# Kernel tuning notes

Hardware: AMD Instinct MI355X
Metric: run time of the kernel (lower is better)

## Reference

```python
import jax, jax.numpy as jnp
import numpy as np

MAX_SEQ_LEN = 2048
H, K = 16, 8
D_IN, D_OUT = 1024, 1024
D_H, D_O = D_IN // H, D_OUT // H


def _get_phi(L, K):
    # Hankel matrix Z[i,j] = 2 / ((i+j)^3 - (i+j) + 1e-7), 1-indexed
    e = np.arange(1, L + 1, dtype=np.float64)
    s = e[:, None] + e[None, :]
    Z = 2.0 / (s ** 3 - s + 1e-7)
    sigma, phi = np.linalg.eigh(Z)
    sigma, phi = sigma[-K:], phi[:, -K:]
    phi = phi * sigma ** 0.25
    return jnp.asarray(phi, dtype=jnp.float32)  # (L, K)


def setup_inputs() -> dict:
    key = jax.random.key(0)
    k_x, k_w, k_d = jax.random.split(key, 3)
    B, T = 4, 2048
    x = jax.random.normal(k_x, (B, T, D_IN), dtype=jnp.float32)
    # kaiming_uniform(a=sqrt(5)) on (H,K,d_h,d_o): fan_in = K*d_h*d_o, bound = 1/sqrt(fan_in)
    fan_in = K * D_H * D_O
    bound = 1.0 / np.sqrt(fan_in)
    weight = jax.random.uniform(k_w, (H, K, D_H, D_O), minval=-bound, maxval=bound, dtype=jnp.float32)
    # torch init is zeros; use small random so the score path is exercised
    diag = 0.02 * jax.random.normal(k_d, (K, D_IN), dtype=jnp.float32)
    phi = _get_phi(MAX_SEQ_LEN, K)
    return {"x": x, "weight": weight, "diag": diag, "phi": phi}


def reference(x, weight, diag, phi):
    B, T, _ = x.shape
    Hh, Kk, d_h, d_o = weight.shape
    # scores: (B, T, K) = phi[:T] broadcast + x @ diag^T
    scores = phi[:T][None, :, :] + jnp.einsum('bti,ki->btk', x, diag)
    xh = x.reshape(B, T, Hh, d_h).transpose(0, 2, 1, 3)  # (B, H, T, d_h)
    # per-head, per-expert GEMM -> (B, H, K, T, d_o)
    y = jnp.einsum('bhti,hkio->bhkto', xh, weight)
    # score-weighted combine over experts -> (B, T, H, d_o)
    y = jnp.einsum('bhkto,btk->btho', y, scores)
    return y.reshape(B, T, Hh * d_o)
```

## Files before the change

kernel.cpp:

```cpp
#include <hip/hip_runtime.h>
#include <hip/hip_bf16.h>

#define BT    8192
#define SEQ_T 2048
#define DIN   1024
#define NH    16
#define NK    8
#define DH    64
#define DO    64

typedef __bf16 bf16;
typedef __attribute__((ext_vector_type(8))) __bf16 bf16x8;
typedef __attribute__((ext_vector_type(4))) __bf16 bf16x4;
typedef __attribute__((ext_vector_type(4))) float floatx4;

__global__ __launch_bounds__(256) void prep_kernel(
    const float* __restrict__ x, const float* __restrict__ weight,
    const float* __restrict__ diag, const float* __restrict__ phi,
    float* __restrict__ scores_t, bf16* __restrict__ wt)
{
  int blk = blockIdx.x, tid = threadIdx.x;
  if (blk < BT / 4) {
    int wave = tid >> 6, lane = tid & 63;
    int token = blk * 4 + wave;
    const floatx4* xr = (const floatx4*)(x + (size_t)token * DIN);
    const floatx4* dg = (const floatx4*)diag;
    floatx4 acc[NK];
#pragma unroll
    for (int k = 0; k < NK; k++) acc[k] = (floatx4){0.f, 0.f, 0.f, 0.f};
#pragma unroll
    for (int it = 0; it < 4; it++) {
      floatx4 xv = xr[it * 64 + lane];
#pragma unroll
      for (int k = 0; k < NK; k++) {
        floatx4 dv = dg[k * 256 + it * 64 + lane];
        acc[k] += xv * dv;
      }
    }
    float r[NK];
#pragma unroll
    for (int k = 0; k < NK; k++)
      r[k] = (acc[k][0] + acc[k][1]) + (acc[k][2] + acc[k][3]);
#pragma unroll
    for (int k = 0; k < NK; k++) {
      float v = r[k];
#pragma unroll
      for (int off = 32; off >= 1; off >>= 1) v += __shfl_xor(v, off, 64);
      r[k] = v;
    }
    if (lane == 0) {
      int t = token & (SEQ_T - 1);
#pragma unroll
      for (int k = 0; k < NK; k++)
        scores_t[(size_t)k * BT + token] = phi[t * NK + k] + r[k];
    }
  } else {
    __shared__ bf16 tile[64 * 68];
    int hk = blk - BT / 4;
    const float* wsrc = weight + (size_t)hk * DH * DO;
#pragma unroll
    for (int it = 0; it < 4; it++) {
      int idx = it * 1024 + tid * 4;
      int i = idx >> 6, o = idx & 63;
      floatx4 v = *(const floatx4*)(wsrc + idx);
#pragma unroll
      for (int r = 0; r < 4; r++)
        tile[(o + r) * 68 + i] = (bf16)v[r];
    }
    __syncthreads();
#pragma unroll
    for (int it = 0; it < 4; it++) {
      int idx = it * 1024 + tid * 4;
      int o2 = idx >> 6, i2 = idx & 63;
      bf16x4 v = *(const bf16x4*)&tile[o2 * 68 + i2];
      *(bf16x4*)(wt + (size_t)hk * 4096 + idx) = v;
    }
  }
}

__global__ __launch_bounds__(256, 3) void moe_kernel(
    const float* __restrict__ x, const bf16* __restrict__ wt,
    const float* __restrict__ scores_t, float* __restrict__ out)
{
  __shared__ bf16  xl[128 * 64];
  __shared__ bf16  wl[256 * 64];
  __shared__ float sl[NK * 128];

  int bid = blockIdx.x;
  int g  = bid >> 5;
  int h  = (bid >> 1) & 15;
  int nh = bid & 1;
  int tid = threadIdx.x, lane = tid & 63, w = tid >> 6;
  int l15 = lane & 15, q = lane >> 4;

  {
    const float* xs = x + (size_t)(g * 128) * DIN + h * 64;
#pragma unroll
    for (int it = 0; it < 4; it++) {
      int idx = it * 256 + tid;
      int row = idx >> 3, c = idx & 7;
      const float* p = xs + (size_t)row * DIN + c * 8;
      floatx4 u0 = *(const floatx4*)p;
      floatx4 u1 = *(const floatx4*)(p + 4);
      bf16x8 v;
      v[0] = (bf16)u0[0]; v[1] = (bf16)u0[1];
      v[2] = (bf16)u0[2]; v[3] = (bf16)u0[3];
      v[4] = (bf16)u1[0]; v[5] = (bf16)u1[1];
      v[6] = (bf16)u1[2]; v[7] = (bf16)u1[3];
      int pc = c ^ (row & 7);
      *(bf16x8*)(xl + row * 64 + pc * 8) = v;
    }
  }
  {
#pragma unroll
    for (int it = 0; it < 8; it++) {
      int idx = it * 256 + tid;
      int R = idx >> 3, c = idx & 7;
      int e = R >> 5, o = R & 31;
      bf16x8 v = *(const bf16x8*)(wt + ((size_t)(h * NK + e) * DO + nh * 32 + o) * 64 + c * 8);
      int pc = c ^ (R & 7);
      *(bf16x8*)(wl + R * 64 + pc * 8) = v;
    }
  }
  {
    int k = tid >> 5, t4 = (tid & 31) * 4;
    floatx4 v = *(const floatx4*)(scores_t + (size_t)k * BT + g * 128 + t4);
    *(floatx4*)(sl + k * 128 + t4) = v;
  }
  __syncthreads();

  int mh = w >> 1;
  int ns = w & 1;

  bf16x8 b[NK][2];
#pragma unroll
  for (int e = 0; e < NK; e++) {
    int R = e * 32 + ns * 16 + l15;
#pragma unroll
    for (int ki = 0; ki < 2; ki++) {
      int pc = (ki * 4 + q) ^ (R & 7);
      b[e][ki] = *(const bf16x8*)(wl + R * 64 + pc * 8);
    }
  }

#pragma unroll
  for (int m = 0; m < 4; m++) {
    int tr = mh * 64 + m * 16;
    int row = tr + l15;
    int p0 = q ^ (row & 7), p1 = (q + 4) ^ (row & 7);
    bf16x8 a0 = *(const bf16x8*)(xl + row * 64 + p0 * 8);
    bf16x8 a1 = *(const bf16x8*)(xl + row * 64 + p1 * 8);
    floatx4 y = (floatx4){0.f, 0.f, 0.f, 0.f};
#pragma unroll
    for (int e = 0; e < NK; e++) {
      floatx4 s4 = *(const floatx4*)(sl + e * 128 + tr + q * 4);
      floatx4 z = (floatx4){0.f, 0.f, 0.f, 0.f};
      z = __builtin_amdgcn_mfma_f32_16x16x32_bf16(a0, b[e][0], z, 0, 0, 0);
      z = __builtin_amdgcn_mfma_f32_16x16x32_bf16(a1, b[e][1], z, 0, 0, 0);
      y += s4 * z;
    }
    int orow = g * 128 + tr + q * 4;
    float* op = out + (size_t)orow * (NH * DO) + h * DO + nh * 32 + ns * 16 + l15;
#pragma unroll
    for (int r = 0; r < 4; r++)
      op[(size_t)r * (NH * DO)] = y[r];
  }
}

extern "C" void kernel_launch(void* const* d_in, const int* in_sizes, int n_in,
                              void* d_out, int out_size, void* d_ws, size_t ws_size,
                              hipStream_t stream) {
  const float* x      = (const float*)d_in[0];
  const float* weight = (const float*)d_in[1];
  const float* diag   = (const float*)d_in[2];
  const float* phi    = (const float*)d_in[3];
  float* out = (float*)d_out;

  bf16*  wt       = (bf16*)d_ws;
  float* scores_t = (float*)((char*)d_ws + (2u << 20));

  prep_kernel<<<BT / 4 + NH * NK, 256, 0, stream>>>(x, weight, diag, phi,
                                                    scores_t, wt);
  moe_kernel<<<64 * NH * 2, 256, 0, stream>>>(x, wt, scores_t, out);
}
```

Before: 110.0 us.

## Fuse prep and MoE kernels into one persistent kernel with grid barrier

Merges the score/weight-prep kernel and the MoE GEMM kernel into one persistent kernel of 768 blocks. Blocks grid-stride over the score tokens and weight-transpose tiles, meet at an atomic-counter grid barrier, then grid-stride over the GEMM tiles. The aim is to remove the second launch and the gap between the kernels. In exchange it adds a memset, a software grid barrier that assumes all 768 blocks are resident at once (256 CUs × 3), and less parallelism in the GEMM phase, since each block now handles about 1.3 tiles sequentially.

```diff
diff --git a/kernel.cpp b/kernel.cpp
--- a/kernel.cpp
+++ b/kernel.cpp
@@ -8,21 +8,43 @@
 #define NK    8
 #define DH    64
 #define DO    64
+#define GRID  768
 
 typedef __bf16 bf16;
 typedef __attribute__((ext_vector_type(8))) __bf16 bf16x8;
 typedef __attribute__((ext_vector_type(4))) __bf16 bf16x4;
 typedef __attribute__((ext_vector_type(4))) float floatx4;
 
-__global__ __launch_bounds__(256) void prep_kernel(
+__device__ __forceinline__ void grid_sync(unsigned* cnt) {
+  __syncthreads();
+  if (threadIdx.x == 0) {
+    __threadfence();
+    unsigned v = __hip_atomic_fetch_add(cnt, 1u, __ATOMIC_ACQ_REL,
+                                        __HIP_MEMORY_SCOPE_AGENT);
+    unsigned target = (v / GRID + 1u) * GRID;
+    while (__hip_atomic_load(cnt, __ATOMIC_ACQUIRE,
+                             __HIP_MEMORY_SCOPE_AGENT) < target)
+      __builtin_amdgcn_s_sleep(2);
+    __threadfence();
+  }
+  __syncthreads();
+}
+
+__global__ __launch_bounds__(256, 3) void fused_kernel(
     const float* __restrict__ x, const float* __restrict__ weight,
     const float* __restrict__ diag, const float* __restrict__ phi,
-    float* __restrict__ scores_t, bf16* __restrict__ wt)
+    bf16* __restrict__ wt, float* __restrict__ scores_t,
+    float* __restrict__ out, unsigned* __restrict__ cnt)
 {
-  int blk = blockIdx.x, tid = threadIdx.x;
-  if (blk < BT / 4) {
-    int wave = tid >> 6, lane = tid & 63;
-    int token = blk * 4 + wave;
+  __shared__ bf16  xl[128 * 64];
+  __shared__ bf16  wl[256 * 64];
+  __shared__ float sl[NK * 128];
+
+  int b = blockIdx.x, tid = threadIdx.x;
+  int wave = tid >> 6, lane = tid & 63;
+
+  for (int tq = b; tq < BT / 4; tq += GRID) {
+    int token = tq * 4 + wave;
     const floatx4* xr = (const floatx4*)(x + (size_t)token * DIN);
     const floatx4* dg = (const floatx4*)diag;
     floatx4 acc[NK];
@@ -54,10 +76,11 @@
       for (int k = 0; k < NK; k++)
         scores_t[(size_t)k * BT + token] = phi[t * NK + k] + r[k];
     }
-  } else {
-    __shared__ bf16 tile[64 * 68];
-    int hk = blk - BT / 4;
-    const float* wsrc = weight + (size_t)hk * DH * DO;
+  }
+
+  if (b < NH * NK) {
+    bf16* tile = wl;
+    const float* wsrc = weight + (size_t)b * DH * DO;
 #pragma unroll
     for (int it = 0; it < 4; it++) {
       int idx = it * 1024 + tid * 4;
@@ -73,97 +96,92 @@
       int idx = it * 1024 + tid * 4;
       int o2 = idx >> 6, i2 = idx & 63;
       bf16x4 v = *(const bf16x4*)&tile[o2 * 68 + i2];
-      *(bf16x4*)(wt + (size_t)hk * 4096 + idx) = v;
-    }
-  }
-}
-
-__global__ __launch_bounds__(256, 3) void moe_kernel(
-    const float* __restrict__ x, const bf16* __restrict__ wt,
-    const float* __restrict__ scores_t, float* __restrict__ out)
-{
-  __shared__ bf16  xl[128 * 64];
-  __shared__ bf16  wl[256 * 64];
-  __shared__ float sl[NK * 128];
-
-  int bid = blockIdx.x;
-  int g  = bid >> 5;
-  int h  = (bid >> 1) & 15;
-  int nh = bid & 1;
-  int tid = threadIdx.x, lane = tid & 63, w = tid >> 6;
-  int l15 = lane & 15, q = lane >> 4;
-
-  {
-    const float* xs = x + (size_t)(g * 128) * DIN + h * 64;
-#pragma unroll
-    for (int it = 0; it < 4; it++) {
-      int idx = it * 256 + tid;
-      int row = idx >> 3, c = idx & 7;
-      const float* p = xs + (size_t)row * DIN + c * 8;
-      floatx4 u0 = *(const floatx4*)p;
-      floatx4 u1 = *(const floatx4*)(p + 4);
-      bf16x8 v;
-      v[0] = (bf16)u0[0]; v[1] = (bf16)u0[1];
-      v[2] = (bf16)u0[2]; v[3] = (bf16)u0[3];
-      v[4] = (bf16)u1[0]; v[5] = (bf16)u1[1];
-      v[6] = (bf16)u1[2]; v[7] = (bf16)u1[3];
-      int pc = c ^ (row & 7);
-      *(bf16x8*)(xl + row * 64 + pc * 8) = v;
-    }
-  }
-  {
-#pragma unroll
-    for (int it = 0; it < 8; it++) {
-      int idx = it * 256 + tid;
-      int R = idx >> 3, c = idx & 7;
-      int e = R >> 5, o = R & 31;
-      bf16x8 v = *(const bf16x8*)(wt + ((size_t)(h * NK + e) * DO + nh * 32 + o) * 64 + c * 8);
-      int pc = c ^ (R & 7);
-      *(bf16x8*)(wl + R * 64 + pc * 8) = v;
-    }
-  }
-  {
-    int k = tid >> 5, t4 = (tid & 31) * 4;
-    floatx4 v = *(const floatx4*)(scores_t + (size_t)k * BT + g * 128 + t4);
-    *(floatx4*)(sl + k * 128 + t4) = v;
-  }
-  __syncthreads();
-
+      *(bf16x4*)(wt + (size_t)b * 4096 + idx) = v;
+    }
+  }
+
+  grid_sync(cnt);
+
+  int l15 = lane & 15, q = lane >> 4, w = tid >> 6;
   int mh = w >> 1;
   int ns = w & 1;
 
-  bf16x8 b[NK][2];
-#pragma unroll
-  for (int e = 0; e < NK; e++) {
-    int R = e * 32 + ns * 16 + l15;
-#pragma unroll
-    for (int ki = 0; ki < 2; ki++) {
-      int pc = (ki * 4 + q) ^ (R & 7);
-      b[e][ki] = *(const bf16x8*)(wl + R * 64 + pc * 8);
-    }
-  }
-
-#pragma unroll
-  for (int m = 0; m < 4; m++) {
-    int tr = mh * 64 + m * 16;
-    int row = tr + l15;
-    int p0 = q ^ (row & 7), p1 = (q + 4) ^ (row & 7);
-    bf16x8 a0 = *(const bf16x8*)(xl + row * 64 + p0 * 8);
-    bf16x8 a1 = *(const bf16x8*)(xl + row * 64 + p1 * 8);
-    floatx4 y = (floatx4){0.f, 0.f, 0.f, 0.f};
+  for (int t5 = b; t5 < 64 * NH * 2; t5 += GRID) {
+    int g  = t5 >> 5;
+    int h  = (t5 >> 1) & 15;
+    int nh = t5 & 1;
+
+    __syncthreads();
+
+    {
+      const float* xs = x + (size_t)(g * 128) * DIN + h * 64;
+#pragma unroll
+      for (int it = 0; it < 4; it++) {
+        int idx = it * 256 + tid;
+        int row = idx >> 3, c = idx & 7;
+        const float* p = xs + (size_t)row * DIN + c * 8;
+        floatx4 u0 = *(const floatx4*)p;
+        floatx4 u1 = *(const floatx4*)(p + 4);
+        bf16x8 v;
+        v[0] = (bf16)u0[0]; v[1] = (bf16)u0[1];
+        v[2] = (bf16)u0[2]; v[3] = (bf16)u0[3];
+        v[4] = (bf16)u1[0]; v[5] = (bf16)u1[1];
+        v[6] = (bf16)u1[2]; v[7] = (bf16)u1[3];
+        int pc = c ^ (row & 7);
+        *(bf16x8*)(xl + row * 64 + pc * 8) = v;
+      }
+    }
+    {
+#pragma unroll
+      for (int it = 0; it < 8; it++) {
+        int idx = it * 256 + tid;
+        int R = idx >> 3, c = idx & 7;
+        int e = R >> 5, o = R & 31;
+        bf16x8 v = *(const bf16x8*)(wt + ((size_t)(h * NK + e) * DO + nh * 32 + o) * 64 + c * 8);
+        int pc = c ^ (R & 7);
+        *(bf16x8*)(wl + R * 64 + pc * 8) = v;
+      }
+    }
+    {
+      int k = tid >> 5, t4 = (tid & 31) * 4;
+      floatx4 v = *(const floatx4*)(scores_t + (size_t)k * BT + g * 128 + t4);
+      *(floatx4*)(sl + k * 128 + t4) = v;
+    }
+    __syncthreads();
+
+    bf16x8 bfr[NK][2];
 #pragma unroll
     for (int e = 0; e < NK; e++) {
-      floatx4 s4 = *(const floatx4*)(sl + e * 128 + tr + q * 4);
-      floatx4 z = (floatx4){0.f, 0.f, 0.f, 0.f};
-      z = __builtin_amdgcn_mfma_f32_16x16x32_bf16(a0, b[e][0], z, 0, 0, 0);
-      z = __builtin_amdgcn_mfma_f32_16x16x32_bf16(a1, b[e][1], z, 0, 0, 0);
-      y += s4 * z;
-    }
-    int orow = g * 128 + tr + q * 4;
-    float* op = out + (size_t)orow * (NH * DO) + h * DO + nh * 32 + ns * 16 + l15;
-#pragma unroll
-    for (int r = 0; r < 4; r++)
-      op[(size_t)r * (NH * DO)] = y[r];
+      int R = e * 32 + ns * 16 + l15;
+#pragma unroll
+      for (int ki = 0; ki < 2; ki++) {
+        int pc = (ki * 4 + q) ^ (R & 7);
+        bfr[e][ki] = *(const bf16x8*)(wl + R * 64 + pc * 8);
+      }
+    }
+
+#pragma unroll
+    for (int m = 0; m < 4; m++) {
+      int tr = mh * 64 + m * 16;
+      int row = tr + l15;
+      int p0 = q ^ (row & 7), p1 = (q + 4) ^ (row & 7);
+      bf16x8 a0 = *(const bf16x8*)(xl + row * 64 + p0 * 8);
+      bf16x8 a1 = *(const bf16x8*)(xl + row * 64 + p1 * 8);
+      floatx4 y = (floatx4){0.f, 0.f, 0.f, 0.f};
+#pragma unroll
+      for (int e = 0; e < NK; e++) {
+        floatx4 s4 = *(const floatx4*)(sl + e * 128 + tr + q * 4);
+        floatx4 z = (floatx4){0.f, 0.f, 0.f, 0.f};
+        z = __builtin_amdgcn_mfma_f32_16x16x32_bf16(a0, bfr[e][0], z, 0, 0, 0);
+        z = __builtin_amdgcn_mfma_f32_16x16x32_bf16(a1, bfr[e][1], z, 0, 0, 0);
+        y += s4 * z;
+      }
+      int orow = g * 128 + tr + q * 4;
+      float* op = out + (size_t)orow * (NH * DO) + h * DO + nh * 32 + ns * 16 + l15;
+#pragma unroll
+      for (int r = 0; r < 4; r++)
+        op[(size_t)r * (NH * DO)] = y[r];
+    }
   }
 }
 
@@ -176,10 +194,11 @@
   const float* phi    = (const float*)d_in[3];
   float* out = (float*)d_out;
 
-  bf16*  wt       = (bf16*)d_ws;
-  float* scores_t = (float*)((char*)d_ws + (2u << 20));
-
-  prep_kernel<<<BT / 4 + NH * NK, 256, 0, stream>>>(x, weight, diag, phi,
-                                                    scores_t, wt);
-  moe_kernel<<<64 * NH * 2, 256, 0, stream>>>(x, wt, scores_t, out);
+  bf16*     wt       = (bf16*)d_ws;
+  float*    scores_t = (float*)((char*)d_ws + (2u << 20));
+  unsigned* cnt      = (unsigned*)((char*)d_ws + (3u << 20));
+
+  hipMemsetAsync(cnt, 0, 64, stream);
+  fused_kernel<<<GRID, 256, 0, stream>>>(x, weight, diag, phi, wt, scores_t,
+                                         out, cnt);
 }
```

Measured after the change: 248.2 us. +125.6%, slower.

## Fuse score computation into MoE kernel and pre-swizzle weights for direct LDS loads

Applied to the files above, without the earlier changes.

Moves the per-token score GEMV out of the prep kernel and into the main kernel, so each block of 64 tokens computes its own scores into shared memory. Each block then loops over four heads and two output halves. The weight image is written in a pre-swizzled layout, which lets it be copied straight into LDS with global_load_lds. This removes the scores round-trip through global memory and the heavy prep pass over x. The cost is that each block now runs serially: the score phase (x is read again here) and then eight sequential weight loads with syncs and no overlap. Only 512 blocks are launched, which lowers parallelism and occupancy.

```diff
diff --git a/kernel.cpp b/kernel.cpp
--- a/kernel.cpp
+++ b/kernel.cpp
@@ -14,156 +14,180 @@
 typedef __attribute__((ext_vector_type(4))) __bf16 bf16x4;
 typedef __attribute__((ext_vector_type(4))) float floatx4;
 
-__global__ __launch_bounds__(256) void prep_kernel(
-    const float* __restrict__ x, const float* __restrict__ weight,
-    const float* __restrict__ diag, const float* __restrict__ phi,
-    float* __restrict__ scores_t, bf16* __restrict__ wt)
+#define GLOAD_LDS16(gp, lp)                                        \
+  __builtin_amdgcn_global_load_lds(                                \
+      (__attribute__((address_space(1))) const void*)(gp),         \
+      (__attribute__((address_space(3))) void*)(lp), 16, 0, 0)
+
+__global__ __launch_bounds__(256) void wtrans_kernel(
+    const float* __restrict__ weight, bf16* __restrict__ wimg)
 {
-  int blk = blockIdx.x, tid = threadIdx.x;
-  if (blk < BT / 4) {
-    int wave = tid >> 6, lane = tid & 63;
-    int token = blk * 4 + wave;
-    const floatx4* xr = (const floatx4*)(x + (size_t)token * DIN);
-    const floatx4* dg = (const floatx4*)diag;
-    floatx4 acc[NK];
-#pragma unroll
-    for (int k = 0; k < NK; k++) acc[k] = (floatx4){0.f, 0.f, 0.f, 0.f};
-#pragma unroll
-    for (int it = 0; it < 4; it++) {
-      floatx4 xv = xr[it * 64 + lane];
-#pragma unroll
-      for (int k = 0; k < NK; k++) {
-        floatx4 dv = dg[k * 256 + it * 64 + lane];
-        acc[k] += xv * dv;
-      }
-    }
-    float r[NK];
-#pragma unroll
-    for (int k = 0; k < NK; k++)
-      r[k] = (acc[k][0] + acc[k][1]) + (acc[k][2] + acc[k][3]);
-#pragma unroll
-    for (int k = 0; k < NK; k++) {
-      float v = r[k];
-#pragma unroll
-      for (int off = 32; off >= 1; off >>= 1) v += __shfl_xor(v, off, 64);
-      r[k] = v;
-    }
-    if (lane == 0) {
-      int t = token & (SEQ_T - 1);
-#pragma unroll
-      for (int k = 0; k < NK; k++)
-        scores_t[(size_t)k * BT + token] = phi[t * NK + k] + r[k];
-    }
-  } else {
-    __shared__ bf16 tile[64 * 68];
-    int hk = blk - BT / 4;
-    const float* wsrc = weight + (size_t)hk * DH * DO;
-#pragma unroll
-    for (int it = 0; it < 4; it++) {
-      int idx = it * 1024 + tid * 4;
-      int i = idx >> 6, o = idx & 63;
-      floatx4 v = *(const floatx4*)(wsrc + idx);
-#pragma unroll
-      for (int r = 0; r < 4; r++)
-        tile[(o + r) * 68 + i] = (bf16)v[r];
-    }
-    __syncthreads();
-#pragma unroll
-    for (int it = 0; it < 4; it++) {
-      int idx = it * 1024 + tid * 4;
-      int o2 = idx >> 6, i2 = idx & 63;
-      bf16x4 v = *(const bf16x4*)&tile[o2 * 68 + i2];
-      *(bf16x4*)(wt + (size_t)hk * 4096 + idx) = v;
-    }
+  __shared__ bf16 tile[64 * 68];
+  int hk = blockIdx.x, tid = threadIdx.x;
+  int h = hk >> 3, k = hk & 7;
+  const float* wsrc = weight + (size_t)hk * DH * DO;
+#pragma unroll
+  for (int it = 0; it < 4; it++) {
+    int idx = it * 1024 + tid * 4;
+    int i = idx >> 6, o = idx & 63;
+    floatx4 v = *(const floatx4*)(wsrc + idx);
+#pragma unroll
+    for (int r = 0; r < 4; r++)
+      tile[(o + r) * 68 + i] = (bf16)v[r];
+  }
+  __syncthreads();
+#pragma unroll
+  for (int it = 0; it < 4; it++) {
+    int idx = it * 1024 + tid * 4;
+    int o2 = idx >> 6, i2 = idx & 63;
+    bf16x4 v = *(const bf16x4*)&tile[o2 * 68 + i2];
+    int nh = o2 >> 5, o = o2 & 31, R = k * 32 + o;
+    int a = (((i2 >> 3) ^ (R & 7)) << 3) + (i2 & 7);
+    *(bf16x4*)(wimg + ((size_t)(h * 2 + nh) * 256 + R) * 64 + a) = v;
   }
 }
 
-__global__ __launch_bounds__(256, 3) void moe_kernel(
-    const float* __restrict__ x, const bf16* __restrict__ wt,
-    const float* __restrict__ scores_t, float* __restrict__ out)
+__global__ __launch_bounds__(256, 2) void fused_kernel(
+    const float* __restrict__ x, const float* __restrict__ diag,
+    const float* __restrict__ phi, const bf16* __restrict__ wimg,
+    float* __restrict__ out)
 {
-  __shared__ bf16  xl[128 * 64];
+  __shared__ bf16  xl[64 * 64];
   __shared__ bf16  wl[256 * 64];
-  __shared__ float sl[NK * 128];
+  __shared__ float sl[NK * 64];
 
   int bid = blockIdx.x;
-  int g  = bid >> 5;
-  int h  = (bid >> 1) & 15;
-  int nh = bid & 1;
+  int lid = ((bid & 7) << 6) | (bid >> 3);
+  int g64 = lid >> 2;
+  int hq  = lid & 3;
   int tid = threadIdx.x, lane = tid & 63, w = tid >> 6;
   int l15 = lane & 15, q = lane >> 4;
 
   {
-    const float* xs = x + (size_t)(g * 128) * DIN + h * 64;
-#pragma unroll
-    for (int it = 0; it < 4; it++) {
-      int idx = it * 256 + tid;
-      int row = idx >> 3, c = idx & 7;
-      const float* p = xs + (size_t)row * DIN + c * 8;
-      floatx4 u0 = *(const floatx4*)p;
-      floatx4 u1 = *(const floatx4*)(p + 4);
-      bf16x8 v;
-      v[0] = (bf16)u0[0]; v[1] = (bf16)u0[1];
-      v[2] = (bf16)u0[2]; v[3] = (bf16)u0[3];
-      v[4] = (bf16)u1[0]; v[5] = (bf16)u1[1];
-      v[6] = (bf16)u1[2]; v[7] = (bf16)u1[3];
-      int pc = c ^ (row & 7);
-      *(bf16x8*)(xl + row * 64 + pc * 8) = v;
-    }
-  }
-  {
-#pragma unroll
-    for (int it = 0; it < 8; it++) {
-      int idx = it * 256 + tid;
-      int R = idx >> 3, c = idx & 7;
-      int e = R >> 5, o = R & 31;
-      bf16x8 v = *(const bf16x8*)(wt + ((size_t)(h * NK + e) * DO + nh * 32 + o) * 64 + c * 8);
-      int pc = c ^ (R & 7);
-      *(bf16x8*)(wl + R * 64 + pc * 8) = v;
-    }
-  }
-  {
-    int k = tid >> 5, t4 = (tid & 31) * 4;
-    floatx4 v = *(const floatx4*)(scores_t + (size_t)k * BT + g * 128 + t4);
-    *(floatx4*)(sl + k * 128 + t4) = v;
+    const floatx4* dg  = (const floatx4*)diag;
+    const floatx4* xr0 = (const floatx4*)(x + (size_t)(g64 * 64 + w * 16) * DIN);
+    floatx4 xv[4];
+#pragma unroll
+    for (int it = 0; it < 4; it++) xv[it] = xr0[it * 64 + lane];
+    for (int s = 0; s < 16; s++) {
+      floatx4 nx[4];
+      if (s < 15) {
+        const floatx4* nr = xr0 + (size_t)(s + 1) * (DIN / 4);
+#pragma unroll
+        for (int it = 0; it < 4; it++) nx[it] = nr[it * 64 + lane];
+      }
+      floatx4 acc[NK];
+#pragma unroll
+      for (int k = 0; k < NK; k++) acc[k] = (floatx4){0.f, 0.f, 0.f, 0.f};
+#pragma unroll
+      for (int it = 0; it < 4; it++) {
+#pragma unroll
+        for (int k = 0; k < NK; k++)
+          acc[k] += xv[it] * dg[k * 256 + it * 64 + lane];
+      }
+      float r[NK];
+#pragma unroll
+      for (int k = 0; k < NK; k++)
+        r[k] = (acc[k][0] + acc[k][1]) + (acc[k][2] + acc[k][3]);
+#pragma unroll
+      for (int k = 0; k < NK; k++) {
+        float v = r[k];
+#pragma unroll
+        for (int off = 32; off >= 1; off >>= 1) v += __shfl_xor(v, off, 64);
+        r[k] = v;
+      }
+      if (lane == 0) {
+        int tl = w * 16 + s;
+        int t = (g64 * 64 + tl) & (SEQ_T - 1);
+#pragma unroll
+        for (int k = 0; k < NK; k++)
+          sl[k * 64 + tl] = phi[t * NK + k] + r[k];
+      }
+      if (s < 15) {
+#pragma unroll
+        for (int it = 0; it < 4; it++) xv[it] = nx[it];
+      }
+    }
   }
   __syncthreads();
 
   int mh = w >> 1;
   int ns = w & 1;
 
-  bf16x8 b[NK][2];
-#pragma unroll
-  for (int e = 0; e < NK; e++) {
-    int R = e * 32 + ns * 16 + l15;
-#pragma unroll
-    for (int ki = 0; ki < 2; ki++) {
-      int pc = (ki * 4 + q) ^ (R & 7);
-      b[e][ki] = *(const bf16x8*)(wl + R * 64 + pc * 8);
-    }
-  }
-
-#pragma unroll
-  for (int m = 0; m < 4; m++) {
-    int tr = mh * 64 + m * 16;
-    int row = tr + l15;
-    int p0 = q ^ (row & 7), p1 = (q + 4) ^ (row & 7);
-    bf16x8 a0 = *(const bf16x8*)(xl + row * 64 + p0 * 8);
-    bf16x8 a1 = *(const bf16x8*)(xl + row * 64 + p1 * 8);
-    floatx4 y = (floatx4){0.f, 0.f, 0.f, 0.f};
+  auto compute_store = [&](int h, int nh) {
+    bf16x8 b[NK][2];
 #pragma unroll
     for (int e = 0; e < NK; e++) {
-      floatx4 s4 = *(const floatx4*)(sl + e * 128 + tr + q * 4);
-      floatx4 z = (floatx4){0.f, 0.f, 0.f, 0.f};
-      z = __builtin_amdgcn_mfma_f32_16x16x32_bf16(a0, b[e][0], z, 0, 0, 0);
-      z = __builtin_amdgcn_mfma_f32_16x16x32_bf16(a1, b[e][1], z, 0, 0, 0);
-      y += s4 * z;
-    }
-    int orow = g * 128 + tr + q * 4;
-    float* op = out + (size_t)orow * (NH * DO) + h * DO + nh * 32 + ns * 16 + l15;
-#pragma unroll
-    for (int r = 0; r < 4; r++)
-      op[(size_t)r * (NH * DO)] = y[r];
+      int R = e * 32 + ns * 16 + l15;
+#pragma unroll
+      for (int ki = 0; ki < 2; ki++) {
+        int pc = (ki * 4 + q) ^ (R & 7);
+        b[e][ki] = *(const bf16x8*)(wl + R * 64 + pc * 8);
+      }
+    }
+#pragma unroll
+    for (int m = 0; m < 2; m++) {
+      int tr = mh * 32 + m * 16;
+      int row = tr + l15;
+      int p0 = q ^ (row & 7), p1 = (q + 4) ^ (row & 7);
+      bf16x8 a0 = *(const bf16x8*)(xl + row * 64 + p0 * 8);
+      bf16x8 a1 = *(const bf16x8*)(xl + row * 64 + p1 * 8);
+      floatx4 y = (floatx4){0.f, 0.f, 0.f, 0.f};
+#pragma unroll
+      for (int e = 0; e < NK; e++) {
+        floatx4 s4 = *(const floatx4*)(sl + e * 64 + tr + q * 4);
+        floatx4 z = (floatx4){0.f, 0.f, 0.f, 0.f};
+        z = __builtin_amdgcn_mfma_f32_16x16x32_bf16(a0, b[e][0], z, 0, 0, 0);
+        z = __builtin_amdgcn_mfma_f32_16x16x32_bf16(a1, b[e][1], z, 0, 0, 0);
+        y += s4 * z;
+      }
+      int orow = g64 * 64 + tr + q * 4;
+      float* op = out + (size_t)orow * (NH * DO) + h * DO + nh * 32
+                      + ns * 16 + l15;
+#pragma unroll
+      for (int r = 0; r < 4; r++)
+        op[(size_t)r * (NH * DO)] = y[r];
+    }
+  };
+
+  for (int hh = 0; hh < 4; hh++) {
+    int h = hq * 4 + hh;
+    if (hh) __syncthreads();
+
+    {
+      const float* xs = x + (size_t)(g64 * 64) * DIN + h * 64;
+#pragma unroll
+      for (int it = 0; it < 2; it++) {
+        int idx = it * 256 + tid;
+        int row = idx >> 3, c = idx & 7;
+        const float* p = xs + (size_t)row * DIN + c * 8;
+        floatx4 u0 = *(const floatx4*)p;
+        floatx4 u1 = *(const floatx4*)(p + 4);
+        bf16x8 v;
+        v[0] = (bf16)u0[0]; v[1] = (bf16)u0[1];
+        v[2] = (bf16)u0[2]; v[3] = (bf16)u0[3];
+        v[4] = (bf16)u1[0]; v[5] = (bf16)u1[1];
+        v[6] = (bf16)u1[2]; v[7] = (bf16)u1[3];
+        *(bf16x8*)(xl + row * 64 + ((c ^ (row & 7)) << 3)) = v;
+      }
+    }
+    {
+      const bf16* ws = wimg + (size_t)(h * 2 + 0) * 16384;
+#pragma unroll
+      for (int it = 0; it < 8; it++)
+        GLOAD_LDS16(ws + it * 2048 + tid * 8, wl + it * 2048 + tid * 8);
+    }
+    __syncthreads();
+    compute_store(h, 0);
+    __syncthreads();
+    {
+      const bf16* ws = wimg + (size_t)(h * 2 + 1) * 16384;
+#pragma unroll
+      for (int it = 0; it < 8; it++)
+        GLOAD_LDS16(ws + it * 2048 + tid * 8, wl + it * 2048 + tid * 8);
+    }
+    __syncthreads();
+    compute_store(h, 1);
   }
 }
 
@@ -176,10 +200,8 @@
   const float* phi    = (const float*)d_in[3];
   float* out = (float*)d_out;
 
-  bf16*  wt       = (bf16*)d_ws;
-  float* scores_t = (float*)((char*)d_ws + (2u << 20));
-
-  prep_kernel<<<BT / 4 + NH * NK, 256, 0, stream>>>(x, weight, diag, phi,
-                                                    scores_t, wt);
-  moe_kernel<<<64 * NH * 2, 256, 0, stream>>>(x, wt, scores_t, out);
+  bf16* wimg = (bf16*)d_ws;
+
+  wtrans_kernel<<<NH * NK, 256, 0, stream>>>(weight, wimg);
+  fused_kernel<<<512, 256, 0, stream>>>(x, diag, phi, wimg, out);
 }
```

After: 119.4 us. 1.09x slower.
